# Kernel tuning notes

Measured on AMD Instinct MI355X. Metric: run time of the kernel, lower is better.

## Reference

```python
import jax, jax.numpy as jnp
import numpy as np

K = 4  # knn_graph(k=4, loop=False) hard-coded in H2GCN.forward


def _knn_2hop_adj(Fet, k):
    """Per-batch kNN graph -> symmetrize -> 2-hop binary adjacency [B,N,N].

    Matches create_adj + get_2hop_neighbors: edge direction and the row
    normalization in create_adj are irrelevant because get_2hop_neighbors
    symmetrizes (adj[row,col]=adj[col,row]=1) and thresholds (adj@adj > 0).
    """
    B, N, _ = Fet.shape
    sq = jnp.sum(Fet * Fet, axis=-1)  # [B,N]
    dist = sq[:, :, None] + sq[:, None, :] - 2.0 * jnp.einsum('bnf,bmf->bnm', Fet, Fet)
    eye = jnp.eye(N, dtype=bool)
    dist = jnp.where(eye[None], jnp.inf, dist)  # loop=False: exclude self
    _, idx = jax.lax.top_k(-dist, k)  # [B,N,k] nearest-neighbor indices
    b_idx = jnp.arange(B)[:, None, None]
    n_idx = jnp.arange(N)[None, :, None]
    A = jnp.zeros((B, N, N), Fet.dtype).at[b_idx, n_idx, idx].set(1.0)
    A = jnp.maximum(A, jnp.swapaxes(A, 1, 2))  # symmetrize 1-hop
    A2 = jnp.einsum('bnm,bmk->bnk', A, A)      # 2-hop counts
    A2 = jnp.where(eye[None], 0.0, A2)          # fill_diagonal_(0)
    return (A2 > 0).astype(Fet.dtype)


def _h2gcn_conv(x, A2, w1, b1, w2, b2):
    """H2GCNConv on dense binary adjacency.

    Dense matmul with binary A2 == gather(x[col]) -> fc2 -> index_add over rows;
    A2.sum(-1) == bincount(row). Degree clamped to >= 1.
    """
    ego = jnp.einsum('bnf,of->bno', x, w1) + b1   # fc1(x)
    msg = jnp.einsum('bnf,of->bno', x, w2) + b2   # fc2(x)
    agg = jnp.einsum('bnm,bmo->bno', A2, msg)     # scatter-add of neighbor msgs
    deg = jnp.maximum(jnp.sum(A2, axis=-1, keepdims=True), 1.0)
    return jax.nn.relu(jnp.concatenate([ego, agg / deg], axis=-1))


def setup_inputs() -> dict:
    key = jax.random.key(0)
    ks = jax.random.split(key, 8)
    B, N, F, NH, NC = 128, 197, 768, 512, 1000
    s = 0.02
    return {
        'Fet': jax.random.normal(ks[0], (B, N, F), jnp.float32),
        'w1_0': jax.random.normal(ks[1], (NH, F), jnp.float32) * s,
        'b1_0': jnp.zeros((NH,), jnp.float32),
        'w2_0': jax.random.normal(ks[2], (NH, F), jnp.float32) * s,
        'b2_0': jnp.zeros((NH,), jnp.float32),
        'w1_1': jax.random.normal(ks[3], (NH, 2 * NH), jnp.float32) * s,
        'b1_1': jnp.zeros((NH,), jnp.float32),
        'w2_1': jax.random.normal(ks[4], (NH, 2 * NH), jnp.float32) * s,
        'b2_1': jnp.zeros((NH,), jnp.float32),
        'fc1_w': jax.random.normal(ks[5], (NH, 4 * NH), jnp.float32) * s,
        'fc1_b': jnp.zeros((NH,), jnp.float32),
        'fc2_w': jax.random.normal(ks[6], (NC, NH), jnp.float32) * s,
        'fc2_b': jnp.zeros((NC,), jnp.float32),
    }


def reference(Fet, w1_0, b1_0, w2_0, b2_0, w1_1, b1_1, w2_1, b2_1,
              fc1_w, fc1_b, fc2_w, fc2_b):
    A2 = _knn_2hop_adj(Fet, K)
    h1 = _h2gcn_conv(Fet, A2, w1_0, b1_0, w2_0, b2_0)   # [B,N,2*nhid]
    h2 = _h2gcn_conv(h1, A2, w1_1, b1_1, w2_1, b2_1)    # [B,N,2*nhid]
    h = jnp.concatenate([h1, h2], axis=-1)              # [B,N,final_dim]
    graph_features = jnp.mean(h, axis=1)                # global_mean_pool
    p = jax.nn.relu(graph_features @ fc1_w.T + fc1_b)   # dropout is identity (eval)
    out = p @ fc2_w.T + fc2_b
    return (out, graph_features)
```

## Files before the change

kernel.cpp:

```cpp
#include <hip/hip_runtime.h>
#include <hip/hip_bf16.h>
#include <math.h>

typedef __attribute__((ext_vector_type(8))) short bf16x8;
typedef __attribute__((ext_vector_type(4))) float f32x4;

#define B_ 128
#define N_ 197
#define F_ 768
#define NH_ 512
#define D2_ 1024
#define D4_ 2048
#define NC_ 1000
#define ROWS_ (B_ * N_)
#define KA_ 224
#define NA_ 256

#define OFF_DIST0  0ull
#define OFF_SQ     19871232ull
#define OFF_ABITS  19972352ull
#define OFF_DEG    20779520ull
#define OFF_FETHI  20880640ull
#define OFF_MSG    59710720ull
#define OFF_H1     85564672ull
#define OFF_FETLO  OFF_MSG
#define OFF_POOL   137338112ull
#define OFF_P      138386688ull
#define OFF_WC1    138648832ull
#define OFF_WC2    140221696ull
#define OFF_DIST1  142318848ull

__device__ __forceinline__ void gll16(const void* g, void* l) {
  __builtin_amdgcn_global_load_lds((const __attribute__((address_space(1))) void*)g,
                                   (__attribute__((address_space(3))) void*)l, 16, 0, 0);
}

__global__ __launch_bounds__(256) void cast_bf16_kernel(const float* __restrict__ src,
                                                        __hip_bfloat16* __restrict__ dst,
                                                        int n4) {
  int i = blockIdx.x * 256 + threadIdx.x;
  if (i >= n4) return;
  float4 v = ((const float4*)src)[i];
  union { __hip_bfloat16 h[4]; uint2 u; } pk;
  pk.h[0] = __float2bfloat16(v.x);
  pk.h[1] = __float2bfloat16(v.y);
  pk.h[2] = __float2bfloat16(v.z);
  pk.h[3] = __float2bfloat16(v.w);
  ((uint2*)dst)[i] = pk.u;
}

__global__ __launch_bounds__(256) void cast_hilo_sq(const float* __restrict__ X,
                                                    __hip_bfloat16* __restrict__ hi,
                                                    __hip_bfloat16* __restrict__ lo,
                                                    float* __restrict__ sq) {
  int row = blockIdx.x * 4 + (threadIdx.x >> 6);
  int lane = threadIdx.x & 63;
  const float4* xp = (const float4*)(X + (size_t)row * F_);
  uint2* hp = (uint2*)(hi + (size_t)row * F_);
  uint2* lp = (uint2*)(lo + (size_t)row * F_);
  float s = 0.f;
#pragma unroll
  for (int i = 0; i < 3; i++) {
    float4 v = xp[lane + i * 64];
    s += v.x * v.x + v.y * v.y + v.z * v.z + v.w * v.w;
    float f[4] = {v.x, v.y, v.z, v.w};
    union { __hip_bfloat16 h[4]; uint2 u; } ph, pl;
#pragma unroll
    for (int k = 0; k < 4; k++) {
      __hip_bfloat16 h = __float2bfloat16(f[k]);
      ph.h[k] = h;
      pl.h[k] = __float2bfloat16(f[k] - __bfloat162float(h));
    }
    hp[lane + i * 64] = ph.u;
    lp[lane + i * 64] = pl.u;
  }
#pragma unroll
  for (int o = 32; o > 0; o >>= 1) s += __shfl_down(s, o);
  if (lane == 0) sq[row] = s;
}

__global__ __launch_bounds__(256) void mfma_gram(const __hip_bfloat16* __restrict__ Xhi,
                                                 const __hip_bfloat16* __restrict__ Xlo,
                                                 float* __restrict__ g0,
                                                 float* __restrict__ g1) {
  __shared__ short AsH[4096];
  __shared__ short BsH[4096];
  __shared__ short AsL[4096];
  __shared__ short BsL[4096];
  const int t = threadIdx.x;
  const int b = blockIdx.z;
  const int bx = blockIdx.x;
  const int khalf = blockIdx.y;
  const int m0 = (bx == 0) ? 0 : 128;
  const int o0 = (bx == 2) ? 128 : 0;
  const bool mirror = (bx == 1);
  const int l = t & 63, w = t >> 6;
  const int wm = (w >> 1) * 64, wn = (w & 1) * 64;
  const int frow = l & 15, fch = l >> 4;
  const int srow = t >> 2, sslot = t & 3;
  const size_t rowbase = (size_t)b * N_;
  const char* AhiB = (const char*)(Xhi + (rowbase + m0) * F_);
  const char* AloB = (const char*)(Xlo + (rowbase + m0) * F_);
  const char* BhiB = (const char*)(Xhi + (rowbase + o0) * F_);
  const char* BloB = (const char*)(Xlo + (rowbase + o0) * F_);
  const int rb = F_ * 2;
  char* AsHB = (char*)AsH;
  char* BsHB = (char*)BsH;
  char* AsLB = (char*)AsL;
  char* BsLB = (char*)BsL;
  float* go = khalf ? g1 : g0;
  f32x4 zero = {0.f, 0.f, 0.f, 0.f};
  f32x4 acc[4][4];
#pragma unroll
  for (int i = 0; i < 4; i++)
#pragma unroll
    for (int j = 0; j < 4; j++) acc[i][j] = zero;
  const int kt0 = khalf * 12;
  for (int kt = kt0; kt < kt0 + 12; kt++) {
    const int kb = kt * 64;
#pragma unroll
    for (int u = 0; u < 2; u++) {
      int grow = u * 64 + srow;
      int gslot = sslot ^ (grow & 3);
      size_t goff = (size_t)grow * rb + kb + gslot * 16;
      gll16(AhiB + goff, AsHB + u * 4096 + t * 16);
      gll16(BhiB + goff, BsHB + u * 4096 + t * 16);
      gll16(AloB + goff, AsLB + u * 4096 + t * 16);
      gll16(BloB + goff, BsLB + u * 4096 + t * 16);
    }
    __syncthreads();
    bf16x8 ah[4], al[4], bh[4], bl[4];
#pragma unroll
    for (int i = 0; i < 4; i++) {
      int ar = wm + i * 16 + frow;
      int aoff = ar * 64 + ((fch ^ (ar & 3)) * 16);
      ah[i] = *(const bf16x8*)(AsHB + aoff);
      al[i] = *(const bf16x8*)(AsLB + aoff);
      int br = wn + i * 16 + frow;
      int boff = br * 64 + ((fch ^ (br & 3)) * 16);
      bh[i] = *(const bf16x8*)(BsHB + boff);
      bl[i] = *(const bf16x8*)(BsLB + boff);
    }
#pragma unroll
    for (int i = 0; i < 4; i++)
#pragma unroll
      for (int j = 0; j < 4; j++) {
        acc[i][j] = __builtin_amdgcn_mfma_f32_16x16x32_bf16(ah[i], bh[j], acc[i][j], 0, 0, 0);
        acc[i][j] = __builtin_amdgcn_mfma_f32_16x16x32_bf16(ah[i], bl[j], acc[i][j], 0, 0, 0);
        acc[i][j] = __builtin_amdgcn_mfma_f32_16x16x32_bf16(al[i], bh[j], acc[i][j], 0, 0, 0);
      }
    __syncthreads();
  }
#pragma unroll
  for (int j = 0; j < 4; j++) {
    int m = o0 + wn + j * 16 + frow;
    if (m >= N_) continue;
#pragma unroll
    for (int i = 0; i < 4; i++) {
      int nb = m0 + wm + i * 16 + fch * 4;
#pragma unroll
      for (int r = 0; r < 4; r++) {
        int n = nb + r;
        if (n >= N_) continue;
        float g = acc[i][j][r];
        go[(rowbase + n) * N_ + m] = g;
        if (mirror) go[(rowbase + m) * N_ + n] = g;
      }
    }
  }
}

__global__ __launch_bounds__(256) void topk_kernel(const float* __restrict__ g0,
                                                   const float* __restrict__ g1,
                                                   const float* __restrict__ sq,
                                                   unsigned long long* __restrict__ Abits) {
  int row = blockIdx.x * 4 + (threadIdx.x >> 6);
  int lane = threadIdx.x & 63;
  int b = row / N_, n = row - b * N_;
  const float* g0r = g0 + (size_t)row * N_;
  const float* g1r = g1 + (size_t)row * N_;
  const float* sqb = sq + (size_t)b * N_;
  float v[4];
  int vi[4];
#pragma unroll
  for (int i = 0; i < 4; i++) {
    int m = lane + i * 64;
    bool ok = (m < N_) && (m != n);
    v[i] = ok ? (sqb[m] - 2.f * (g0r[m] + g1r[m])) : INFINITY;
    vi[i] = ok ? m : 0x3fffffff;
  }
  unsigned long long nbr[4] = {0ull, 0ull, 0ull, 0ull};
#pragma unroll
  for (int t = 0; t < 4; t++) {
    float bv = v[0];
    int bi = vi[0];
#pragma unroll
    for (int i = 1; i < 4; i++)
      if (v[i] < bv || (v[i] == bv && vi[i] < bi)) { bv = v[i]; bi = vi[i]; }
#pragma unroll
    for (int o = 1; o < 64; o <<= 1) {
      float ov = __shfl_xor(bv, o);
      int oi = __shfl_xor(bi, o);
      if (ov < bv || (ov == bv && oi < bi)) { bv = ov; bi = oi; }
    }
#pragma unroll
    for (int i = 0; i < 4; i++)
      if (vi[i] == bi) { v[i] = INFINITY; vi[i] = 0x3fffffff; }
    if (lane == 0) {
      nbr[bi >> 6] |= 1ull << (bi & 63);
      atomicOr(&Abits[((size_t)b * N_ + bi) * 4 + (n >> 6)], 1ull << (n & 63));
    }
  }
  if (lane == 0) {
#pragma unroll
    for (int w = 0; w < 4; w++)
      if (nbr[w]) atomicOr(&Abits[(size_t)row * 4 + w], nbr[w]);
  }
}

__global__ __launch_bounds__(256) void a2_kernel(const unsigned long long* __restrict__ Abits,
                                                 __hip_bfloat16* __restrict__ A2bf,
                                                 float* __restrict__ deg) {
  int row = blockIdx.x * 4 + (threadIdx.x >> 6);
  int lane = threadIdx.x & 63;
  int b = row / N_, n = row - b * N_;
  const unsigned long long* arow = Abits + (size_t)row * 4;
  const unsigned long long* base = Abits + (size_t)b * N_ * 4;
  unsigned long long r0 = 0, r1 = 0, r2 = 0, r3 = 0;
#pragma unroll
  for (int w = 0; w < 4; w++) {
    if ((arow[w] >> lane) & 1ull) {
      const unsigned long long* mr = base + (size_t)(w * 64 + lane) * 4;
      r0 |= mr[0]; r1 |= mr[1]; r2 |= mr[2]; r3 |= mr[3];
    }
  }
#pragma unroll
  for (int o = 1; o < 64; o <<= 1) {
    r0 |= __shfl_xor(r0, o);
    r1 |= __shfl_xor(r1, o);
    r2 |= __shfl_xor(r2, o);
    r3 |= __shfl_xor(r3, o);
  }
  unsigned long long rr[4] = {r0, r1, r2, r3};
  rr[n >> 6] &= ~(1ull << (n & 63));
  __hip_bfloat16* out = A2bf + ((size_t)b * NA_ + n) * KA_;
  const __hip_bfloat16 one = __float2bfloat16(1.f);
  const __hip_bfloat16 zer = __float2bfloat16(0.f);
#pragma unroll
  for (int i = 0; i < 4; i++) {
    int m = lane + i * 64;
    if (m < KA_)
      out[m] = (m < N_ && ((rr[m >> 6] >> (m & 63)) & 1ull)) ? one : zer;
  }
  if (lane == 0) {
    int dg = __popcll(rr[0]) + __popcll(rr[1]) + __popcll(rr[2]) + __popcll(rr[3]);
    deg[row] = (float)(dg > 0 ? dg : 1);
  }
}

template <int MODE>
__global__ __launch_bounds__(256) void mfma_fused(const __hip_bfloat16* __restrict__ X,
                                                  const __hip_bfloat16* __restrict__ Wcat,
                                                  const float* __restrict__ biasE,
                                                  const float* __restrict__ biasM,
                                                  __hip_bfloat16* __restrict__ h1,
                                                  __hip_bfloat16* __restrict__ msg,
                                                  float* __restrict__ pool,
                                                  int K) {
  __shared__ short As[4096];
  __shared__ short Bs[4096];
  const int t = threadIdx.x;
  const int m0 = blockIdx.y * 128, o0 = blockIdx.x * 128;
  const int l = t & 63, w = t >> 6;
  const int wm = (w >> 1) * 64, wn = (w & 1) * 64;
  const int frow = l & 15, fch = l >> 4;
  const int srow = t >> 2, sslot = t & 3;
  const char* Abase = (const char*)(X + (size_t)m0 * K);
  const char* Bbase = (const char*)(Wcat + (size_t)o0 * K);
  const int rb = K * 2;
  char* AsB = (char*)As;
  char* BsB = (char*)Bs;
  f32x4 zero = {0.f, 0.f, 0.f, 0.f};
  f32x4 acc[4][4];
#pragma unroll
  for (int i = 0; i < 4; i++)
#pragma unroll
    for (int j = 0; j < 4; j++) acc[i][j] = zero;
  const int KT = K >> 5;
  for (int kt = 0; kt < KT; kt++) {
    const int kb = kt * 64;
#pragma unroll
    for (int u = 0; u < 2; u++) {
      int grow = u * 64 + srow;
      int gslot = sslot ^ (grow & 3);
      gll16(Abase + (size_t)grow * rb + kb + gslot * 16, AsB + u * 4096 + t * 16);
      gll16(Bbase + (size_t)grow * rb + kb + gslot * 16, BsB + u * 4096 + t * 16);
    }
    __syncthreads();
    bf16x8 af[4], bfv[4];
#pragma unroll
    for (int i = 0; i < 4; i++) {
      int ar = wm + i * 16 + frow;
      af[i] = *(const bf16x8*)(AsB + ar * 64 + ((fch ^ (ar & 3)) * 16));
      int br = wn + i * 16 + frow;
      bfv[i] = *(const bf16x8*)(BsB + br * 64 + ((fch ^ (br & 3)) * 16));
    }
#pragma unroll
    for (int i = 0; i < 4; i++)
#pragma unroll
      for (int j = 0; j < 4; j++)
        acc[i][j] = __builtin_amdgcn_mfma_f32_16x16x32_bf16(af[i], bfv[j], acc[i][j], 0, 0, 0);
    __syncthreads();
  }
  const bool ego = (o0 < 512);
#pragma unroll
  for (int j = 0; j < 4; j++) {
    int c = o0 + wn + j * 16 + frow;
    if (ego) {
      float bv = biasE[c];
      if (MODE == 1) {
#pragma unroll
        for (int i = 0; i < 4; i++) {
          int r0 = m0 + wm + i * 16 + fch * 4;
#pragma unroll
          for (int r = 0; r < 4; r++) {
            float v = fmaxf(acc[i][j][r] + bv, 0.f);
            h1[(size_t)(r0 + r) * D2_ + c] = __float2bfloat16(v);
          }
        }
      } else {
        int rw = m0 + wm;
        int b0 = rw / N_;
        int rB = (b0 + 1) * N_;
        float sA = 0.f, sB = 0.f;
#pragma unroll
        for (int i = 0; i < 4; i++) {
          int r0 = m0 + wm + i * 16 + fch * 4;
#pragma unroll
          for (int r = 0; r < 4; r++) {
            float v = fmaxf(acc[i][j][r] + bv, 0.f);
            if (r0 + r < rB) sA += v; else sB += v;
          }
        }
        sA += __shfl_down(sA, 32);
        sA += __shfl_down(sA, 16);
        sB += __shfl_down(sB, 32);
        sB += __shfl_down(sB, 16);
        if (l < 16) {
          atomicAdd(&pool[(size_t)b0 * D4_ + D2_ + c], sA);
          if (rw + 64 > rB) atomicAdd(&pool[(size_t)(b0 + 1) * D4_ + D2_ + c], sB);
        }
      }
    } else {
      float bv = biasM[c - 512];
#pragma unroll
      for (int i = 0; i < 4; i++) {
        int r0 = m0 + wm + i * 16 + fch * 4;
#pragma unroll
        for (int r = 0; r < 4; r++)
          msg[(size_t)(r0 + r) * NH_ + (c - 512)] = __float2bfloat16(acc[i][j][r] + bv);
      }
    }
  }
}

template <int MODE>
__global__ __launch_bounds__(256) void mfma_agg(const __hip_bfloat16* __restrict__ A2bf,
                                                const __hip_bfloat16* __restrict__ msg,
                                                const float* __restrict__ deg,
                                                __hip_bfloat16* __restrict__ H,
                                                float* __restrict__ pool, int poolOff) {
  __shared__ short As[4096];
  __shared__ short Bs[4096];
  const int t = threadIdx.x;
  const int b = blockIdx.z;
  const int m0 = blockIdx.y * 128, o0 = blockIdx.x * 128;
  const int l = t & 63, w = t >> 6;
  const int wm = (w >> 1) * 64, wn = (w & 1) * 64;
  const int frow = l & 15, fch = l >> 4;
  const int srow = t >> 2, sslot = t & 3;
  const char* Abase = (const char*)(A2bf + ((size_t)b * NA_ + m0) * KA_);
  const __hip_bfloat16* Mb = msg + (size_t)b * N_ * NH_;
  const int bk = t >> 3;
  const int bf0 = (t & 7) * 16;
  char* AsB = (char*)As;
  char* BsB = (char*)Bs;
  f32x4 zero = {0.f, 0.f, 0.f, 0.f};
  f32x4 acc[4][4];
#pragma unroll
  for (int i = 0; i < 4; i++)
#pragma unroll
    for (int j = 0; j < 4; j++) acc[i][j] = zero;
  for (int kt = 0; kt < 7; kt++) {
#pragma unroll
    for (int u = 0; u < 2; u++) {
      int grow = u * 64 + srow;
      int gslot = sslot ^ (grow & 3);
      gll16(Abase + (size_t)grow * (KA_ * 2) + kt * 64 + gslot * 16, AsB + u * 4096 + t * 16);
    }
    int krow = kt * 32 + bk;
    const __hip_bfloat16* mp = Mb + (size_t)krow * NH_ + o0 + bf0;
    bf16x8 v0 = *(const bf16x8*)mp;
    bf16x8 v1 = *(const bf16x8*)(mp + 8);
#pragma unroll
    for (int e = 0; e < 8; e++) {
      int f0a = bf0 + e;
      int f1a = bf0 + 8 + e;
      *(short*)(BsB + f0a * 64 + (((bk >> 3) ^ (f0a & 3)) * 16) + (bk & 7) * 2) = v0[e];
      *(short*)(BsB + f1a * 64 + (((bk >> 3) ^ (f1a & 3)) * 16) + (bk & 7) * 2) = v1[e];
    }
    __syncthreads();
    bf16x8 af[4], bfv[4];
#pragma unroll
    for (int i = 0; i < 4; i++) {
      int ar = wm + i * 16 + frow;
      af[i] = *(const bf16x8*)(AsB + ar * 64 + ((fch ^ (ar & 3)) * 16));
      int br = wn + i * 16 + frow;
      bfv[i] = *(const bf16x8*)(BsB + br * 64 + ((fch ^ (br & 3)) * 16));
    }
#pragma unroll
    for (int i = 0; i < 4; i++)
#pragma unroll
      for (int j = 0; j < 4; j++)
        acc[i][j] = __builtin_amdgcn_mfma_f32_16x16x32_bf16(af[i], bfv[j], acc[i][j], 0, 0, 0);
    __syncthreads();
  }
#pragma unroll
  for (int j = 0; j < 4; j++) {
    int c = o0 + wn + j * 16 + frow;
    float s = 0.f;
#pragma unroll
    for (int i = 0; i < 4; i++) {
#pragma unroll
      for (int r = 0; r < 4; r++) {
        int n = m0 + wm + i * 16 + fch * 4 + r;
        if (n < N_) {
          float dv = deg[b * N_ + n];
          float v = fmaxf(acc[i][j][r] / dv, 0.f);
          if (MODE == 0)
            H[((size_t)b * N_ + n) * D2_ + NH_ + c] = __float2bfloat16(v);
          s += v;
        }
      }
    }
    s += __shfl_down(s, 32);
    s += __shfl_down(s, 16);
    if (l < 16) atomicAdd(&pool[(size_t)b * D4_ + poolOff + c], s);
  }
}

__global__ __launch_bounds__(256) void pool_h1ego(const __hip_bfloat16* __restrict__ h1,
                                                  float* __restrict__ gf) {
  int b = blockIdx.y;
  int c = blockIdx.x * 256 + threadIdx.x;
  const __hip_bfloat16* p = h1 + (size_t)b * N_ * D2_ + c;
  float s = 0.f;
  for (int n = 0; n < N_; n++) s += __bfloat162float(p[(size_t)n * D2_]);
  gf[(size_t)b * D4_ + c] = s * (1.f / N_);
}

__global__ __launch_bounds__(256) void scale_pool(const float* __restrict__ pool,
                                                  float* __restrict__ gf) {
  int b = blockIdx.y;
  int c = NH_ + blockIdx.x * 256 + threadIdx.x;
  gf[(size_t)b * D4_ + c] = pool[(size_t)b * D4_ + c] * (1.f / N_);
}

template <bool RELUX>
__global__ __launch_bounds__(256) void head_gemm(const float* __restrict__ Xg,
                                                 const float* __restrict__ W,
                                                 const float* __restrict__ bias,
                                                 float* __restrict__ Y,
                                                 int Rows, int Fin, int O, int kchunk) {
  __shared__ float Xs[16][68];
  __shared__ float Ws[16][68];
  int tx = threadIdx.x, ty = threadIdx.y;
  int tid = ty * 16 + tx;
  int lr = tid >> 2;
  int lk = (tid & 3) * 4;
  int rbase = blockIdx.y * 64;
  int o0 = blockIdx.x * 64;
  int k0base = blockIdx.z * kchunk;
  float acc[4][4] = {};
  for (int k0 = k0base; k0 < k0base + kchunk; k0 += 16) {
    float4 xv = make_float4(0.f, 0.f, 0.f, 0.f);
    if (rbase + lr < Rows) xv = *(const float4*)&Xg[(size_t)(rbase + lr) * Fin + k0 + lk];
    if (RELUX) {
      xv.x = fmaxf(xv.x, 0.f); xv.y = fmaxf(xv.y, 0.f);
      xv.z = fmaxf(xv.z, 0.f); xv.w = fmaxf(xv.w, 0.f);
    }
    Xs[lk][lr] = xv.x; Xs[lk + 1][lr] = xv.y; Xs[lk + 2][lr] = xv.z; Xs[lk + 3][lr] = xv.w;
    float4 wv = make_float4(0.f, 0.f, 0.f, 0.f);
    if (o0 + lr < O) wv = *(const float4*)&W[(size_t)(o0 + lr) * Fin + k0 + lk];
    Ws[lk][lr] = wv.x; Ws[lk + 1][lr] = wv.y; Ws[lk + 2][lr] = wv.z; Ws[lk + 3][lr] = wv.w;
    __syncthreads();
#pragma unroll
    for (int k = 0; k < 16; k++) {
      float4 a = *(const float4*)&Xs[k][ty * 4];
      float4 bb = *(const float4*)&Ws[k][tx * 4];
      float av[4] = {a.x, a.y, a.z, a.w};
      float bv[4] = {bb.x, bb.y, bb.z, bb.w};
#pragma unroll
      for (int i = 0; i < 4; i++)
#pragma unroll
        for (int j = 0; j < 4; j++) acc[i][j] = fmaf(av[i], bv[j], acc[i][j]);
    }
    __syncthreads();
  }
#pragma unroll
  for (int i = 0; i < 4; i++) {
    int rrow = rbase + ty * 4 + i;
    if (rrow >= Rows) continue;
#pragma unroll
    for (int j = 0; j < 4; j++) {
      int c = o0 + tx * 4 + j;
      if (c >= O) continue;
      float vv = acc[i][j] + ((blockIdx.z == 0) ? bias[c] : 0.f);
      atomicAdd(&Y[(size_t)rrow * O + c], vv);
    }
  }
}

extern "C" void kernel_launch(void* const* d_in, const int* in_sizes, int n_in,
                              void* d_out, int out_size, void* d_ws, size_t ws_size,
                              hipStream_t stream) {
  const float* Fet  = (const float*)d_in[0];
  const float* w1_0 = (const float*)d_in[1];
  const float* b1_0 = (const float*)d_in[2];
  const float* w2_0 = (const float*)d_in[3];
  const float* b2_0 = (const float*)d_in[4];
  const float* w1_1 = (const float*)d_in[5];
  const float* b1_1 = (const float*)d_in[6];
  const float* w2_1 = (const float*)d_in[7];
  const float* b2_1 = (const float*)d_in[8];
  const float* fc1_w = (const float*)d_in[9];
  const float* fc1_b = (const float*)d_in[10];
  const float* fc2_w = (const float*)d_in[11];
  const float* fc2_b = (const float*)d_in[12];

  char* ws = (char*)d_ws;
  float* g0 = (float*)(ws + OFF_DIST0);
  float* g1 = (float*)(ws + OFF_DIST1);
  __hip_bfloat16* A2bf = (__hip_bfloat16*)(ws + OFF_DIST0);
  float* sq = (float*)(ws + OFF_SQ);
  unsigned long long* Abits = (unsigned long long*)(ws + OFF_ABITS);
  float* deg = (float*)(ws + OFF_DEG);
  __hip_bfloat16* Fet_hi = (__hip_bfloat16*)(ws + OFF_FETHI);
  __hip_bfloat16* Fet_lo = (__hip_bfloat16*)(ws + OFF_FETLO);
  __hip_bfloat16* msg = (__hip_bfloat16*)(ws + OFF_MSG);
  __hip_bfloat16* h1 = (__hip_bfloat16*)(ws + OFF_H1);
  float* pool = (float*)(ws + OFF_POOL);
  float* p = (float*)(ws + OFF_P);
  __hip_bfloat16* wc1 = (__hip_bfloat16*)(ws + OFF_WC1);
  __hip_bfloat16* wc2 = (__hip_bfloat16*)(ws + OFF_WC2);

  float* out = (float*)d_out;
  float* gf = out + (size_t)B_ * NC_;

  hipMemsetAsync(Abits, 0, (size_t)ROWS_ * 4 * sizeof(unsigned long long), stream);
  hipMemsetAsync(pool, 0, (size_t)B_ * D4_ * sizeof(float), stream);
  hipMemsetAsync(p, 0, (size_t)B_ * NH_ * sizeof(float), stream);
  hipMemsetAsync(out, 0, (size_t)B_ * NC_ * sizeof(float), stream);

  cast_hilo_sq<<<ROWS_ / 4, 256, 0, stream>>>(Fet, Fet_hi, Fet_lo, sq);
  cast_bf16_kernel<<<384, 256, 0, stream>>>(w1_0, wc1, NH_ * F_ / 4);
  cast_bf16_kernel<<<384, 256, 0, stream>>>(w2_0, wc1 + (size_t)NH_ * F_, NH_ * F_ / 4);
  cast_bf16_kernel<<<512, 256, 0, stream>>>(w1_1, wc2, NH_ * D2_ / 4);
  cast_bf16_kernel<<<512, 256, 0, stream>>>(w2_1, wc2 + (size_t)NH_ * D2_, NH_ * D2_ / 4);

  mfma_gram<<<dim3(3, 2, B_), 256, 0, stream>>>(Fet_hi, Fet_lo, g0, g1);
  topk_kernel<<<ROWS_ / 4, 256, 0, stream>>>(g0, g1, sq, Abits);
  a2_kernel<<<ROWS_ / 4, 256, 0, stream>>>(Abits, A2bf, deg);

  mfma_fused<1><<<dim3(8, 197), 256, 0, stream>>>(
      Fet_hi, wc1, b1_0, b2_0, h1, msg, nullptr, F_);
  mfma_agg<0><<<dim3(4, 2, B_), 256, 0, stream>>>(A2bf, msg, deg, h1, pool, NH_);

  mfma_fused<2><<<dim3(8, 197), 256, 0, stream>>>(
      h1, wc2, b1_1, b2_1, nullptr, msg, pool, D2_);
  mfma_agg<1><<<dim3(4, 2, B_), 256, 0, stream>>>(A2bf, msg, deg, nullptr, pool, D2_ + NH_);

  pool_h1ego<<<dim3(2, B_), 256, 0, stream>>>(h1, gf);
  scale_pool<<<dim3(6, B_), 256, 0, stream>>>(pool, gf);

  head_gemm<false><<<dim3(8, 2, 16), dim3(16, 16), 0, stream>>>(
      gf, fc1_w, fc1_b, p, B_, D4_, NH_, 128);
  head_gemm<true><<<dim3(16, 2, 8), dim3(16, 16), 0, stream>>>(
      p, fc2_w, fc2_b, out, B_, NH_, NC_, 64);
}
```

Measured before the change: 535.6 us.

## Store messages transposed for async LDS loads, remap workgroups, widen LDS swizzle

The message GEMM now writes its output transposed per batch (msgT, padded to KA_ columns) by swapping MFMA operand order for the message half. The aggregation kernel can then stream B tiles with direct global-to-LDS loads instead of per-element scalar LDS scatter. Workgroup IDs in the gram, fused and aggregation kernels are remapped with an XCD-aware interleave (wgid&7) to improve L2 locality across the chiplets. The LDS XOR swizzle also mixes in row bits 2-3 to reduce bank conflicts. The transposed stores are strided 2-byte writes, which may cost write bandwidth in the fused kernel.

Result: no change. 525.2 us (-1.9%).

```diff
diff --git a/kernel.cpp b/kernel.cpp
--- a/kernel.cpp
+++ b/kernel.cpp
@@ -21,19 +21,21 @@
 #define OFF_ABITS  19972352ull
 #define OFF_DEG    20779520ull
 #define OFF_FETHI  20880640ull
-#define OFF_MSG    59710720ull
-#define OFF_H1     85564672ull
-#define OFF_FETLO  OFF_MSG
-#define OFF_POOL   137338112ull
-#define OFF_P      138386688ull
-#define OFF_WC1    138648832ull
-#define OFF_WC2    140221696ull
-#define OFF_DIST1  142318848ull
+#define OFF_MSGT   59710720ull
+#define OFF_H1     89070848ull
+#define OFF_FETLO  OFF_MSGT
+#define OFF_POOL   140844288ull
+#define OFF_P      141892864ull
+#define OFF_WC1    142155008ull
+#define OFF_WC2    143727872ull
+#define OFF_DIST1  145825024ull
 
 __device__ __forceinline__ void gll16(const void* g, void* l) {
   __builtin_amdgcn_global_load_lds((const __attribute__((address_space(1))) void*)g,
                                    (__attribute__((address_space(3))) void*)l, 16, 0, 0);
 }
+
+__device__ __forceinline__ int slot_of(int row) { return (row & 3) ^ ((row >> 2) & 3); }
 
 __global__ __launch_bounds__(256) void cast_bf16_kernel(const float* __restrict__ src,
                                                         __hip_bfloat16* __restrict__ dst,
@@ -88,9 +90,12 @@
   __shared__ short AsL[4096];
   __shared__ short BsL[4096];
   const int t = threadIdx.x;
-  const int b = blockIdx.z;
-  const int bx = blockIdx.x;
-  const int khalf = blockIdx.y;
+  const int wgid = blockIdx.x;
+  const int L = (wgid & 7) * 96 + (wgid >> 3);
+  const int b = L / 6;
+  const int rbx = L - b * 6;
+  const int bx = rbx % 3;
+  const int khalf = rbx / 3;
   const int m0 = (bx == 0) ? 0 : 128;
   const int o0 = (bx == 2) ? 128 : 0;
   const bool mirror = (bx == 1);
@@ -121,7 +126,7 @@
 #pragma unroll
     for (int u = 0; u < 2; u++) {
       int grow = u * 64 + srow;
-      int gslot = sslot ^ (grow & 3);
+      int gslot = sslot ^ slot_of(grow);
       size_t goff = (size_t)grow * rb + kb + gslot * 16;
       gll16(AhiB + goff, AsHB + u * 4096 + t * 16);
       gll16(BhiB + goff, BsHB + u * 4096 + t * 16);
@@ -133,11 +138,11 @@
 #pragma unroll
     for (int i = 0; i < 4; i++) {
       int ar = wm + i * 16 + frow;
-      int aoff = ar * 64 + ((fch ^ (ar & 3)) * 16);
+      int aoff = ar * 64 + ((fch ^ slot_of(ar)) * 16);
       ah[i] = *(const bf16x8*)(AsHB + aoff);
       al[i] = *(const bf16x8*)(AsLB + aoff);
       int br = wn + i * 16 + frow;
-      int boff = br * 64 + ((fch ^ (br & 3)) * 16);
+      int boff = br * 64 + ((fch ^ slot_of(br)) * 16);
       bh[i] = *(const bf16x8*)(BsHB + boff);
       bl[i] = *(const bf16x8*)(BsLB + boff);
     }
@@ -264,13 +269,15 @@
                                                   const float* __restrict__ biasE,
                                                   const float* __restrict__ biasM,
                                                   __hip_bfloat16* __restrict__ h1,
-                                                  __hip_bfloat16* __restrict__ msg,
+                                                  __hip_bfloat16* __restrict__ msgT,
                                                   float* __restrict__ pool,
                                                   int K) {
   __shared__ short As[4096];
   __shared__ short Bs[4096];
   const int t = threadIdx.x;
-  const int m0 = blockIdx.y * 128, o0 = blockIdx.x * 128;
+  const int wgid = blockIdx.x;
+  const int L = (wgid & 7) * 197 + (wgid >> 3);
+  const int m0 = (L >> 3) * 128, o0 = (L & 7) * 128;
   const int l = t & 63, w = t >> 6;
   const int wm = (w >> 1) * 64, wn = (w & 1) * 64;
   const int frow = l & 15, fch = l >> 4;
@@ -280,6 +287,7 @@
   const int rb = K * 2;
   char* AsB = (char*)As;
   char* BsB = (char*)Bs;
+  const bool swap = (o0 >= 512);
   f32x4 zero = {0.f, 0.f, 0.f, 0.f};
   f32x4 acc[4][4];
 #pragma unroll
@@ -292,7 +300,7 @@
 #pragma unroll
     for (int u = 0; u < 2; u++) {
       int grow = u * 64 + srow;
-      int gslot = sslot ^ (grow & 3);
+      int gslot = sslot ^ slot_of(grow);
       gll16(Abase + (size_t)grow * rb + kb + gslot * 16, AsB + u * 4096 + t * 16);
       gll16(Bbase + (size_t)grow * rb + kb + gslot * 16, BsB + u * 4096 + t * 16);
     }
@@ -301,22 +309,29 @@
 #pragma unroll
     for (int i = 0; i < 4; i++) {
       int ar = wm + i * 16 + frow;
-      af[i] = *(const bf16x8*)(AsB + ar * 64 + ((fch ^ (ar & 3)) * 16));
+      af[i] = *(const bf16x8*)(AsB + ar * 64 + ((fch ^ slot_of(ar)) * 16));
       int br = wn + i * 16 + frow;
-      bfv[i] = *(const bf16x8*)(BsB + br * 64 + ((fch ^ (br & 3)) * 16));
-    }
-#pragma unroll
-    for (int i = 0; i < 4; i++)
-#pragma unroll
-      for (int j = 0; j < 4; j++)
-        acc[i][j] = __builtin_amdgcn_mfma_f32_16x16x32_bf16(af[i], bfv[j], acc[i][j], 0, 0, 0);
-    __syncthreads();
-  }
-  const bool ego = (o0 < 512);
-#pragma unroll
-  for (int j = 0; j < 4; j++) {
-    int c = o0 + wn + j * 16 + frow;
-    if (ego) {
+      bfv[i] = *(const bf16x8*)(BsB + br * 64 + ((fch ^ slot_of(br)) * 16));
+    }
+    if (!swap) {
+#pragma unroll
+      for (int i = 0; i < 4; i++)
+#pragma unroll
+        for (int j = 0; j < 4; j++)
+          acc[i][j] = __builtin_amdgcn_mfma_f32_16x16x32_bf16(af[i], bfv[j], acc[i][j], 0, 0, 0);
+    } else {
+#pragma unroll
+      for (int i = 0; i < 4; i++)
+#pragma unroll
+        for (int j = 0; j < 4; j++)
+          acc[i][j] = __builtin_amdgcn_mfma_f32_16x16x32_bf16(bfv[j], af[i], acc[i][j], 0, 0, 0);
+    }
+    __syncthreads();
+  }
+  if (!swap) {
+#pragma unroll
+    for (int j = 0; j < 4; j++) {
+      int c = o0 + wn + j * 16 + frow;
       float bv = biasE[c];
       if (MODE == 1) {
 #pragma unroll
@@ -351,14 +366,22 @@
           if (rw + 64 > rB) atomicAdd(&pool[(size_t)(b0 + 1) * D4_ + D2_ + c], sB);
         }
       }
-    } else {
-      float bv = biasM[c - 512];
-#pragma unroll
-      for (int i = 0; i < 4; i++) {
-        int r0 = m0 + wm + i * 16 + fch * 4;
-#pragma unroll
-        for (int r = 0; r < 4; r++)
-          msg[(size_t)(r0 + r) * NH_ + (c - 512)] = __float2bfloat16(acc[i][j][r] + bv);
+    }
+  } else {
+#pragma unroll
+    for (int i = 0; i < 4; i++) {
+      int xrow = m0 + wm + i * 16 + frow;
+      int bb = xrow / N_;
+      int rr = xrow - bb * N_;
+      __hip_bfloat16* mt = msgT + (size_t)bb * NH_ * KA_ + rr;
+#pragma unroll
+      for (int j = 0; j < 4; j++) {
+#pragma unroll
+        for (int r = 0; r < 4; r++) {
+          int cm = (o0 - 512) + wn + j * 16 + fch * 4 + r;
+          float v = acc[i][j][r] + biasM[cm];
+          mt[(size_t)cm * KA_] = __float2bfloat16(v);
+        }
       }
     }
   }
@@ -366,23 +389,25 @@
 
 template <int MODE>
 __global__ __launch_bounds__(256) void mfma_agg(const __hip_bfloat16* __restrict__ A2bf,
-                                                const __hip_bfloat16* __restrict__ msg,
+                                                const __hip_bfloat16* __restrict__ msgT,
                                                 const float* __restrict__ deg,
                                                 __hip_bfloat16* __restrict__ H,
                                                 float* __restrict__ pool, int poolOff) {
   __shared__ short As[4096];
   __shared__ short Bs[4096];
   const int t = threadIdx.x;
-  const int b = blockIdx.z;
-  const int m0 = blockIdx.y * 128, o0 = blockIdx.x * 128;
+  const int wgid = blockIdx.x;
+  const int L = (wgid & 7) * 128 + (wgid >> 3);
+  const int b = L >> 3;
+  const int o0 = ((L >> 1) & 3) * 128;
+  const int m0 = (L & 1) * 128;
   const int l = t & 63, w = t >> 6;
   const int wm = (w >> 1) * 64, wn = (w & 1) * 64;
   const int frow = l & 15, fch = l >> 4;
   const int srow = t >> 2, sslot = t & 3;
   const char* Abase = (const char*)(A2bf + ((size_t)b * NA_ + m0) * KA_);
-  const __hip_bfloat16* Mb = msg + (size_t)b * N_ * NH_;
-  const int bk = t >> 3;
-  const int bf0 = (t & 7) * 16;
+  const char* Bbase = (const char*)(msgT + ((size_t)b * NH_ + o0) * KA_);
+  const int rb = KA_ * 2;
   char* AsB = (char*)As;
   char* BsB = (char*)Bs;
   f32x4 zero = {0.f, 0.f, 0.f, 0.f};
@@ -392,31 +417,22 @@
 #pragma unroll
     for (int j = 0; j < 4; j++) acc[i][j] = zero;
   for (int kt = 0; kt < 7; kt++) {
+    const int kb = kt * 64;
 #pragma unroll
     for (int u = 0; u < 2; u++) {
       int grow = u * 64 + srow;
-      int gslot = sslot ^ (grow & 3);
-      gll16(Abase + (size_t)grow * (KA_ * 2) + kt * 64 + gslot * 16, AsB + u * 4096 + t * 16);
-    }
-    int krow = kt * 32 + bk;
-    const __hip_bfloat16* mp = Mb + (size_t)krow * NH_ + o0 + bf0;
-    bf16x8 v0 = *(const bf16x8*)mp;
-    bf16x8 v1 = *(const bf16x8*)(mp + 8);
-#pragma unroll
-    for (int e = 0; e < 8; e++) {
-      int f0a = bf0 + e;
-      int f1a = bf0 + 8 + e;
-      *(short*)(BsB + f0a * 64 + (((bk >> 3) ^ (f0a & 3)) * 16) + (bk & 7) * 2) = v0[e];
-      *(short*)(BsB + f1a * 64 + (((bk >> 3) ^ (f1a & 3)) * 16) + (bk & 7) * 2) = v1[e];
+      int gslot = sslot ^ slot_of(grow);
+      gll16(Abase + (size_t)grow * rb + kb + gslot * 16, AsB + u * 4096 + t * 16);
+      gll16(Bbase + (size_t)grow * rb + kb + gslot * 16, BsB + u * 4096 + t * 16);
     }
     __syncthreads();
     bf16x8 af[4], bfv[4];
 #pragma unroll
     for (int i = 0; i < 4; i++) {
       int ar = wm + i * 16 + frow;
-      af[i] = *(const bf16x8*)(AsB + ar * 64 + ((fch ^ (ar & 3)) * 16));
+      af[i] = *(const bf16x8*)(AsB + ar * 64 + ((fch ^ slot_of(ar)) * 16));
       int br = wn + i * 16 + frow;
-      bfv[i] = *(const bf16x8*)(BsB + br * 64 + ((fch ^ (br & 3)) * 16));
+      bfv[i] = *(const bf16x8*)(BsB + br * 64 + ((fch ^ slot_of(br)) * 16));
     }
 #pragma unroll
     for (int i = 0; i < 4; i++)
@@ -547,7 +563,7 @@
   float* deg = (float*)(ws + OFF_DEG);
   __hip_bfloat16* Fet_hi = (__hip_bfloat16*)(ws + OFF_FETHI);
   __hip_bfloat16* Fet_lo = (__hip_bfloat16*)(ws + OFF_FETLO);
-  __hip_bfloat16* msg = (__hip_bfloat16*)(ws + OFF_MSG);
+  __hip_bfloat16* msgT = (__hip_bfloat16*)(ws + OFF_MSGT);
   __hip_bfloat16* h1 = (__hip_bfloat16*)(ws + OFF_H1);
   float* pool = (float*)(ws + OFF_POOL);
   float* p = (float*)(ws + OFF_P);
@@ -568,17 +584,15 @@
   cast_bf16_kernel<<<512, 256, 0, stream>>>(w1_1, wc2, NH_ * D2_ / 4);
   cast_bf16_kernel<<<512, 256, 0, stream>>>(w2_1, wc2 + (size_t)NH_ * D2_, NH_ * D2_ / 4);
 
-  mfma_gram<<<dim3(3, 2, B_), 256, 0, stream>>>(Fet_hi, Fet_lo, g0, g1);
+  mfma_gram<<<768, 256, 0, stream>>>(Fet_hi, Fet_lo, g0, g1);
   topk_kernel<<<ROWS_ / 4, 256, 0, stream>>>(g0, g1, sq, Abits);
   a2_kernel<<<ROWS_ / 4, 256, 0, stream>>>(Abits, A2bf, deg);
 
-  mfma_fused<1><<<dim3(8, 197), 256, 0, stream>>>(
-      Fet_hi, wc1, b1_0, b2_0, h1, msg, nullptr, F_);
-  mfma_agg<0><<<dim3(4, 2, B_), 256, 0, stream>>>(A2bf, msg, deg, h1, pool, NH_);
-
-  mfma_fused<2><<<dim3(8, 197), 256, 0, stream>>>(
-      h1, wc2, b1_1, b2_1, nullptr, msg, pool, D2_);
-  mfma_agg<1><<<dim3(4, 2, B_), 256, 0, stream>>>(A2bf, msg, deg, nullptr, pool, D2_ + NH_);
+  mfma_fused<1><<<1576, 256, 0, stream>>>(Fet_hi, wc1, b1_0, b2_0, h1, msgT, nullptr, F_);
+  mfma_agg<0><<<1024, 256, 0, stream>>>(A2bf, msgT, deg, h1, pool, NH_);
+
+  mfma_fused<2><<<1576, 256, 0, stream>>>(h1, wc2, b1_1, b2_1, nullptr, msgT, pool, D2_);
+  mfma_agg<1><<<1024, 256, 0, stream>>>(A2bf, msgT, deg, nullptr, pool, D2_ + NH_);
 
   pool_h1ego<<<dim3(2, B_), 256, 0, stream>>>(h1, gf);
   scale_pool<<<dim3(6, B_), 256, 0, stream>>>(pool, gf);
```
